# Kernel tuning notes

Measured on AMD Instinct MI355X. Metric: run time of the kernel, lower is better.

## Reference

```python
import jax
import jax.numpy as jnp
import numpy as np
from jax import lax

B, L, A, C = 32, 128, 64, 128  # batch, length, n_agents, channels (in == out)
KT = 3                          # temporal kernel size, padding (KT-1)//2 keeps length


def setup_inputs() -> dict:
    key = jax.random.key(0)
    k1, k2, k3 = jax.random.split(key, 3)
    x = jax.random.normal(k1, (B, L, A, C), dtype=jnp.float32)
    # Conv2d weight [out_ch, in_ch, kt, 1] and bias, kaiming-ish scale
    W = jax.random.normal(k2, (C, C, KT, 1), dtype=jnp.float32) * (1.0 / np.sqrt(C * KT))
    b = jax.random.normal(k3, (C,), dtype=jnp.float32) * 0.01
    return {"x": x, "W": W, "b": b}


def reference(x, W, b):
    # x: [B, L, A, C] -> [B, C, L, A] (torch NCHW layout with H=time, W=agents)
    length, n_agents = x.shape[1], x.shape[2]
    xc = jnp.transpose(x, (0, 3, 1, 2))
    res = xc  # residual is identity (input_dim == output_dim, t_stride == 1)
    pad_t = (KT - 1) // 2
    y = lax.conv_general_dilated(
        xc, W,
        window_strides=(1, 1),
        padding=[(pad_t, pad_t), (0, 0)],
        dimension_numbers=("NCHW", "OIHW", "NCHW"),
    ) + b[None, :, None, None]  # [B, C, L, A]
    # Dense graph g[t,a,t',a'] = 1 iff t==t' or a==a'.  einsum('ncv,vw->ncw', x, g)
    # is exactly: sum over same time (all agents) + sum over same agent (all times) - self.
    agent_sum = jnp.sum(y, axis=3, keepdims=True)  # [B, C, L, 1]
    time_sum = jnp.sum(y, axis=2, keepdims=True)   # [B, C, 1, A]
    scale = (length + n_agents - 2) ** 0.5
    g = (agent_sum + time_sum - y) / scale
    out = jax.nn.relu(g + res)
    return jnp.transpose(out, (0, 2, 3, 1))  # [B, L, A, C]
```

## Files before the change

kernel.cpp:

```cpp
#include <hip/hip_runtime.h>
#include <hip/hip_bf16.h>
#include <stdint.h>


typedef __attribute__((ext_vector_type(8))) short bf16x8;
typedef __attribute__((ext_vector_type(4))) float f32x4;

__device__ __forceinline__ uint32_t f2bf(float f) {
    union { __hip_bfloat16 b; uint16_t u; } cv;
    cv.b = __float2bfloat16(f);
    return (uint32_t)cv.u;
}
__device__ __forceinline__ float bf2f(uint32_t h) {
    union { uint32_t u; float f; } v; v.u = h << 16; return v.f;
}
__device__ __forceinline__ uint32_t pk2(float lo, float hi) {
    union { __hip_bfloat162 b; uint32_t u; } cv;
    cv.b = __float22bfloat162_rn(make_float2(lo, hi));
    return cv.u;
}

__global__ __launch_bounds__(256) void red_kernel(
    const float* __restrict__ x, uint16_t* __restrict__ xa16, float* __restrict__ xt_part,
    const float* __restrict__ W, uint16_t* __restrict__ wp)
{
    const int tid = threadIdx.x;
    const int bid = blockIdx.x;
    if (bid >= 512) {
        int o = (bid - 512) * 256 + tid;
        int i = o & 7, lane = (o >> 3) & 63, nt = (o >> 9) & 7, ks = (o >> 12) & 3, d = o >> 14;
        int ci = ks * 32 + (lane >> 4) * 8 + i;
        int co = nt * 16 + (lane & 15);
        wp[o] = (uint16_t)f2bf(W[(co * 128 + ci) * 3 + d]);
        return;
    }
    const int b = bid >> 4, g = bid & 15;
    const int ci8 = (tid & 15) * 8, ag = tid >> 4;
    __shared__ float red[16][128];

    float xtl[4][8];
    #pragma unroll
    for (int r = 0; r < 4; ++r)
        #pragma unroll
        for (int j = 0; j < 8; ++j) xtl[r][j] = 0.f;

    #pragma unroll
    for (int ti = 0; ti < 8; ++ti) {
        const int t = g * 8 + ti;
        const float* xr = x + ((size_t)(b * 128 + t) * 64) * 128;
        float s[8];
        #pragma unroll
        for (int j = 0; j < 8; ++j) s[j] = 0.f;
        #pragma unroll
        for (int r = 0; r < 4; ++r) {
            const int a = ag * 4 + r;
            const float4 v0 = *(const float4*)(xr + a * 128 + ci8);
            const float4 v1 = *(const float4*)(xr + a * 128 + ci8 + 4);
            s[0] += v0.x; s[1] += v0.y; s[2] += v0.z; s[3] += v0.w;
            s[4] += v1.x; s[5] += v1.y; s[6] += v1.z; s[7] += v1.w;
            xtl[r][0] += v0.x; xtl[r][1] += v0.y; xtl[r][2] += v0.z; xtl[r][3] += v0.w;
            xtl[r][4] += v1.x; xtl[r][5] += v1.y; xtl[r][6] += v1.z; xtl[r][7] += v1.w;
        }
        *(float4*)&red[ag][ci8]     = make_float4(s[0], s[1], s[2], s[3]);
        *(float4*)&red[ag][ci8 + 4] = make_float4(s[4], s[5], s[6], s[7]);
        __syncthreads();
        if (tid < 128) {
            float v = 0.f;
            #pragma unroll
            for (int i = 0; i < 16; ++i) v += red[i][tid];
            xa16[(size_t)(b * 130 + t + 1) * 128 + tid] = (uint16_t)f2bf(v);
        }
        __syncthreads();
    }
    if (g == 0 && tid < 16)
        *(uint4*)(xa16 + (size_t)(b * 130) * 128 + tid * 8) = make_uint4(0, 0, 0, 0);
    if (g == 15 && tid < 16)
        *(uint4*)(xa16 + (size_t)(b * 130 + 129) * 128 + tid * 8) = make_uint4(0, 0, 0, 0);
    #pragma unroll
    for (int r = 0; r < 4; ++r) {
        float* p = xt_part + (((size_t)(b * 16 + g) * 64 + ag * 4 + r) * 128) + ci8;
        *(float4*)p       = make_float4(xtl[r][0], xtl[r][1], xtl[r][2], xtl[r][3]);
        *(float4*)(p + 4) = make_float4(xtl[r][4], xtl[r][5], xtl[r][6], xtl[r][7]);
    }
}

__global__ __launch_bounds__(256) void xtr_kernel(
    const float* __restrict__ xt_part, float* __restrict__ xt)
{
    const int idx = blockIdx.x * 256 + threadIdx.x;
    const int row = idx >> 4, ci8 = (idx & 15) * 8;
    const int b = row >> 6, a = row & 63;
    float s[8];
    #pragma unroll
    for (int j = 0; j < 8; ++j) s[j] = 0.f;
    #pragma unroll
    for (int g2 = 0; g2 < 16; ++g2) {
        const float* p = xt_part + (((size_t)(b * 16 + g2) * 64 + a) * 128) + ci8;
        const float4 v0 = *(const float4*)p;
        const float4 v1 = *(const float4*)(p + 4);
        s[0] += v0.x; s[1] += v0.y; s[2] += v0.z; s[3] += v0.w;
        s[4] += v1.x; s[5] += v1.y; s[6] += v1.z; s[7] += v1.w;
    }
    float* q = xt + (size_t)row * 128 + ci8;
    *(float4*)q       = make_float4(s[0], s[1], s[2], s[3]);
    *(float4*)(q + 4) = make_float4(s[4], s[5], s[6], s[7]);
}

__global__ __launch_bounds__(256, 2) void sums_kernel(
    const uint16_t* __restrict__ xa16, const float* __restrict__ xt,
    const float* __restrict__ x, const uint16_t* __restrict__ wp,
    const float* __restrict__ bias, float* __restrict__ asum, float* __restrict__ tsum)
{
    __shared__ __align__(16) uint16_t slab[130 * 128];
    const int tid = threadIdx.x;
    const int lane = tid & 63, wid = tid >> 6;
    const int wm = wid >> 1, wn = wid & 1;
    const int lr = lane & 15, lg = lane >> 4;
    f32x4 acc[4][4];
    #pragma unroll
    for (int mi = 0; mi < 4; ++mi)
        #pragma unroll
        for (int ni = 0; ni < 4; ++ni) acc[mi][ni] = (f32x4)0.f;

    if (blockIdx.x < 32) {
        const int b = blockIdx.x;
        #pragma unroll
        for (int it = 0; it < 9; ++it) {
            const int gg = it * 256 + tid;
            if (gg < 2080) {
                const int row = gg >> 4, sp = gg & 15;
                const int sl = sp ^ (row & 7);
                *(uint4*)(slab + gg * 8) =
                    *(const uint4*)(xa16 + (size_t)(b * 130 + row) * 128 + sl * 8);
            }
        }
        __syncthreads();
        #pragma unroll
        for (int g = 0; g < 4; ++g)
            #pragma unroll
            for (int d = 0; d < 3; ++d) {
                bf16x8 bq[4], af[4];
                #pragma unroll
                for (int ni = 0; ni < 4; ++ni)
                    bq[ni] = *(const bf16x8*)(wp + (size_t)((((d * 4 + g) * 8) + wn * 4 + ni) * 64 + lane) * 8);
                #pragma unroll
                for (int mi = 0; mi < 4; ++mi) {
                    const int row = wm * 64 + mi * 16 + lr + d;
                    af[mi] = *(const bf16x8*)(slab + row * 128 + ((g * 4 + lg) ^ (row & 7)) * 8);
                }
                #pragma unroll
                for (int mi = 0; mi < 4; ++mi)
                    #pragma unroll
                    for (int ni = 0; ni < 4; ++ni)
                        acc[mi][ni] = __builtin_amdgcn_mfma_f32_16x16x32_bf16(af[mi], bq[ni], acc[mi][ni], 0, 0, 0);
            }
        #pragma unroll
        for (int ni = 0; ni < 4; ++ni) {
            const int col = wn * 64 + ni * 16 + lr;
            const float bv = 64.f * bias[col];
            #pragma unroll
            for (int mi = 0; mi < 4; ++mi)
                #pragma unroll
                for (int j = 0; j < 4; ++j) {
                    const int t = wm * 64 + mi * 16 + lg * 4 + j;
                    asum[((size_t)b * 128 + t) * 128 + col] = acc[mi][ni][j] + bv;
                }
        }
        return;
    }

    const int bid = blockIdx.x - 32;
    const int r = tid >> 1, h = tid & 1;
    const int grow = bid * 128 + r, sb = grow >> 6, sa = grow & 63;
    #pragma unroll
    for (int d = 0; d < 3; ++d) {
        {
            const float* Sp = xt + (size_t)grow * 128 + h * 64;
            const float* Ep = x + ((size_t)((sb * 128 + (d == 0 ? 127 : 0)) * 64 + sa)) * 128 + h * 64;
            #pragma unroll
            for (int k = 0; k < 8; ++k) {
                float4 f0 = *(const float4*)(Sp + k * 8);
                float4 f1 = *(const float4*)(Sp + k * 8 + 4);
                if (d != 1) {
                    const float4 e0 = *(const float4*)(Ep + k * 8);
                    const float4 e1 = *(const float4*)(Ep + k * 8 + 4);
                    f0.x -= e0.x; f0.y -= e0.y; f0.z -= e0.z; f0.w -= e0.w;
                    f1.x -= e1.x; f1.y -= e1.y; f1.z -= e1.z; f1.w -= e1.w;
                }
                uint4 o;
                o.x = pk2(f0.x, f0.y); o.y = pk2(f0.z, f0.w);
                o.z = pk2(f1.x, f1.y); o.w = pk2(f1.z, f1.w);
                const int sl = h * 8 + k;
                *(uint4*)(slab + r * 128 + (sl ^ (r & 7)) * 8) = o;
            }
        }
        __syncthreads();
        #pragma unroll
        for (int g = 0; g < 4; ++g) {
            bf16x8 bq[4], af[4];
            #pragma unroll
            for (int ni = 0; ni < 4; ++ni)
                bq[ni] = *(const bf16x8*)(wp + (size_t)((((d * 4 + g) * 8) + wn * 4 + ni) * 64 + lane) * 8);
            #pragma unroll
            for (int mi = 0; mi < 4; ++mi) {
                const int row = wm * 64 + mi * 16 + lr;
                af[mi] = *(const bf16x8*)(slab + row * 128 + ((g * 4 + lg) ^ (row & 7)) * 8);
            }
            #pragma unroll
            for (int mi = 0; mi < 4; ++mi)
                #pragma unroll
                for (int ni = 0; ni < 4; ++ni)
                    acc[mi][ni] = __builtin_amdgcn_mfma_f32_16x16x32_bf16(af[mi], bq[ni], acc[mi][ni], 0, 0, 0);
        }
        __syncthreads();
    }
    #pragma unroll
    for (int ni = 0; ni < 4; ++ni) {
        const int col = wn * 64 + ni * 16 + lr;
        const float bv = 128.f * bias[col];
        #pragma unroll
        for (int mi = 0; mi < 4; ++mi)
            #pragma unroll
            for (int j = 0; j < 4; ++j) {
                const int rg = bid * 128 + wm * 64 + mi * 16 + lg * 4 + j;
                tsum[(size_t)rg * 128 + col] = acc[mi][ni][j] + bv;
            }
    }
}

__global__ __launch_bounds__(512, 6) void conv_kernel(
    const float* __restrict__ x, const uint16_t* __restrict__ wp,
    const float* __restrict__ bias, const float* __restrict__ asum,
    const float* __restrict__ tsum, float* __restrict__ out)
{
    __shared__ __align__(16) uint16_t slab[2][192 * 64];
    const int tid = threadIdx.x;
    const int raw = blockIdx.x;
    const int bid = (raw & 7) * 512 + (raw >> 3);
    const int b = bid >> 7, t = bid & 127;
    const int lane = tid & 63, wid = tid >> 6;
    const int lr = lane & 15, lg = lane >> 4;

    f32x4 acc[4];
    #pragma unroll
    for (int mi = 0; mi < 4; ++mi) acc[mi] = (f32x4)0.f;

#define STAGE(c) do {                                                          \
    _Pragma("unroll")                                                          \
    for (int k = 0; k < 3; ++k) {                                              \
        const int ro  = lane >> 3;                                             \
        const int row = wid * 24 + k * 8 + ro;                                 \
        const int gl  = (lane & 7) ^ ro;                                       \
        const int tloc = t + (row >> 6) - 1;                                   \
        uint4 o4 = make_uint4(0, 0, 0, 0);                                     \
        if ((unsigned)tloc < 128u) {                                           \
            const float* s_ = x +                                              \
                ((size_t)((b * 128 + tloc) * 64 + (row & 63))) * 128 +         \
                (c) * 64 + gl * 8;                                             \
            const float4 v0 = *(const float4*)s_;                              \
            const float4 v1 = *(const float4*)(s_ + 4);                        \
            o4.x = pk2(v0.x, v0.y); o4.y = pk2(v0.z, v0.w);                    \
            o4.z = pk2(v1.x, v1.y); o4.w = pk2(v1.z, v1.w);                    \
        }                                                                      \
        *(uint4*)(&slab[c][wid * 1536 + k * 512 + lane * 8]) = o4;             \
    } } while (0)

#define MFMA_CHUNK(c) do {                                                     \
    _Pragma("unroll")                                                          \
    for (int d = 0; d < 3; ++d)                                                \
        _Pragma("unroll")                                                      \
        for (int g2 = 0; g2 < 2; ++g2) {                                       \
            const int ks = (c) * 2 + g2;                                       \
            bf16x8 bq, af[4];                                                  \
            bq = *(const bf16x8*)(wp +                                         \
                (size_t)((((d * 4 + ks) * 8) + wid) * 64 + lane) * 8);         \
            _Pragma("unroll")                                                  \
            for (int mi = 0; mi < 4; ++mi) {                                   \
                const int row = d * 64 + mi * 16 + lr;                         \
                af[mi] = *(const bf16x8*)(&slab[c][row * 64 +                  \
                    (((g2 * 4 + lg) ^ (row & 7)) * 8)]);                       \
            }                                                                  \
            _Pragma("unroll")                                                  \
            for (int mi = 0; mi < 4; ++mi)                                     \
                acc[mi] = __builtin_amdgcn_mfma_f32_16x16x32_bf16(             \
                    af[mi], bq, acc[mi], 0, 0, 0);                             \
        } } while (0)

    STAGE(0);
    __syncthreads();
    STAGE(1);
    MFMA_CHUNK(0);
    __syncthreads();
    MFMA_CHUNK(1);
    __syncthreads();

#undef STAGE
#undef MFMA_CHUNK

    {
        const int col = wid * 16 + lr;
        const float bv = bias[col];
        const int cbuf = col >> 6, cl = col & 63;
        #pragma unroll
        for (int mi = 0; mi < 4; ++mi)
            #pragma unroll
            for (int j = 0; j < 4; ++j) {
                const int a = mi * 16 + lg * 4 + j;
                slab[cbuf][a * 64 + (cl ^ ((a & 7) << 3))] = (uint16_t)f2bf(acc[mi][j] + bv);
            }
    }
    __syncthreads();

    {
        const float inv = 0.07254762501100116f;
        const int cg = tid & 15, rb = tid >> 4;
        const int cbuf = cg >> 3, cl8 = (cg & 7) * 8;
        const float* ap = asum + ((size_t)(b * 128 + t)) * 128 + cg * 8;
        const float4 as0 = *(const float4*)ap, as1 = *(const float4*)(ap + 4);
        const float av[8] = {as0.x, as0.y, as0.z, as0.w, as1.x, as1.y, as1.z, as1.w};
        #pragma unroll
        for (int j = 0; j < 2; ++j) {
            const int a = j * 32 + rb;
            const int swz = cl8 ^ ((a & 7) << 3);
            const uint4 yv = *(const uint4*)(&slab[cbuf][a * 64 + swz]);
            const uint4 xv = *(const uint4*)(&slab[cbuf][(64 + a) * 64 + swz]);
            const float* tp = tsum + ((size_t)(b * 64 + a)) * 128 + cg * 8;
            const float4 ts0 = *(const float4*)tp, ts1 = *(const float4*)(tp + 4);
            float yy[8], xx[8];
            yy[0] = bf2f(yv.x & 0xFFFFu); yy[1] = bf2f(yv.x >> 16);
            yy[2] = bf2f(yv.y & 0xFFFFu); yy[3] = bf2f(yv.y >> 16);
            yy[4] = bf2f(yv.z & 0xFFFFu); yy[5] = bf2f(yv.z >> 16);
            yy[6] = bf2f(yv.w & 0xFFFFu); yy[7] = bf2f(yv.w >> 16);
            xx[0] = bf2f(xv.x & 0xFFFFu); xx[1] = bf2f(xv.x >> 16);
            xx[2] = bf2f(xv.y & 0xFFFFu); xx[3] = bf2f(xv.y >> 16);
            xx[4] = bf2f(xv.z & 0xFFFFu); xx[5] = bf2f(xv.z >> 16);
            xx[6] = bf2f(xv.w & 0xFFFFu); xx[7] = bf2f(xv.w >> 16);
            const float tv[8] = {ts0.x, ts0.y, ts0.z, ts0.w, ts1.x, ts1.y, ts1.z, ts1.w};
            float o[8];
            #pragma unroll
            for (int i = 0; i < 8; ++i) {
                const float gg = (av[i] + tv[i] - yy[i]) * inv + xx[i];
                o[i] = gg > 0.f ? gg : 0.f;
            }
            float* op = out + ((size_t)((b * 128 + t) * 64 + a)) * 128 + cg * 8;
            *(float4*)op       = make_float4(o[0], o[1], o[2], o[3]);
            *(float4*)(op + 4) = make_float4(o[4], o[5], o[6], o[7]);
        }
    }
}

extern "C" void kernel_launch(void* const* d_in, const int* in_sizes, int n_in,
                              void* d_out, int out_size, void* d_ws, size_t ws_size,
                              hipStream_t stream) {
    const float* x    = (const float*)d_in[0];
    const float* W    = (const float*)d_in[1];
    const float* bias = (const float*)d_in[2];
    float* out = (float*)d_out;

    char* ws = (char*)d_ws;
    uint16_t* wp    = (uint16_t*)(ws);
    uint16_t* xa16  = (uint16_t*)(ws + 98304);
    float* xt_part  = (float*)(ws + 98304 + 1064960);
    float* xt       = (float*)(ws + 98304 + 1064960 + 16777216);
    float* asum     = (float*)(ws + 98304 + 1064960 + 16777216 + 1048576);
    float* tsum     = (float*)(ws + 98304 + 1064960 + 16777216 + 1048576 + 2097152);

    red_kernel  <<<704,  256, 0, stream>>>(x, xa16, xt_part, W, wp);
    xtr_kernel  <<<128,  256, 0, stream>>>(xt_part, xt);
    sums_kernel <<<48,   256, 0, stream>>>(xa16, xt, x, wp, bias, asum, tsum);
    conv_kernel <<<4096, 512, 0, stream>>>(x, wp, bias, asum, tsum, out);
}
```

Measured before the change: 109.8 us.

## Compute agent sums inside conv kernel and halve its LDS footprint

Drops the separate agent-sum path: the per-time reduction in red_kernel and the 32 MFMA blocks in sums_kernel go away. conv_kernel now gets the agent sum for each (b,t) by reducing its own accumulators across lanes with shuffles, writing it to a small shared array. The double-buffered LDS slab becomes a single buffer, with staging and MFMA serialized, so occupancy can rise from 6 to 8. The residual for the first channel half is reread from global x at full precision, because its bf16 copy has been overwritten. Serializing stage and compute gives up the overlap between loads and MFMA.

```diff
diff --git a/kernel.cpp b/kernel.cpp
--- a/kernel.cpp
+++ b/kernel.cpp
@@ -21,7 +21,7 @@
 }
 
 __global__ __launch_bounds__(256) void red_kernel(
-    const float* __restrict__ x, uint16_t* __restrict__ xa16, float* __restrict__ xt_part,
+    const float* __restrict__ x, float* __restrict__ xt_part,
     const float* __restrict__ W, uint16_t* __restrict__ wp)
 {
     const int tid = threadIdx.x;
@@ -36,7 +36,6 @@
     }
     const int b = bid >> 4, g = bid & 15;
     const int ci8 = (tid & 15) * 8, ag = tid >> 4;
-    __shared__ float red[16][128];
 
     float xtl[4][8];
     #pragma unroll
@@ -48,34 +47,15 @@
     for (int ti = 0; ti < 8; ++ti) {
         const int t = g * 8 + ti;
         const float* xr = x + ((size_t)(b * 128 + t) * 64) * 128;
-        float s[8];
-        #pragma unroll
-        for (int j = 0; j < 8; ++j) s[j] = 0.f;
         #pragma unroll
         for (int r = 0; r < 4; ++r) {
             const int a = ag * 4 + r;
             const float4 v0 = *(const float4*)(xr + a * 128 + ci8);
             const float4 v1 = *(const float4*)(xr + a * 128 + ci8 + 4);
-            s[0] += v0.x; s[1] += v0.y; s[2] += v0.z; s[3] += v0.w;
-            s[4] += v1.x; s[5] += v1.y; s[6] += v1.z; s[7] += v1.w;
             xtl[r][0] += v0.x; xtl[r][1] += v0.y; xtl[r][2] += v0.z; xtl[r][3] += v0.w;
             xtl[r][4] += v1.x; xtl[r][5] += v1.y; xtl[r][6] += v1.z; xtl[r][7] += v1.w;
         }
-        *(float4*)&red[ag][ci8]     = make_float4(s[0], s[1], s[2], s[3]);
-        *(float4*)&red[ag][ci8 + 4] = make_float4(s[4], s[5], s[6], s[7]);
-        __syncthreads();
-        if (tid < 128) {
-            float v = 0.f;
-            #pragma unroll
-            for (int i = 0; i < 16; ++i) v += red[i][tid];
-            xa16[(size_t)(b * 130 + t + 1) * 128 + tid] = (uint16_t)f2bf(v);
-        }
-        __syncthreads();
-    }
-    if (g == 0 && tid < 16)
-        *(uint4*)(xa16 + (size_t)(b * 130) * 128 + tid * 8) = make_uint4(0, 0, 0, 0);
-    if (g == 15 && tid < 16)
-        *(uint4*)(xa16 + (size_t)(b * 130 + 129) * 128 + tid * 8) = make_uint4(0, 0, 0, 0);
+    }
     #pragma unroll
     for (int r = 0; r < 4; ++r) {
         float* p = xt_part + (((size_t)(b * 16 + g) * 64 + ag * 4 + r) * 128) + ci8;
@@ -107,11 +87,11 @@
 }
 
 __global__ __launch_bounds__(256, 2) void sums_kernel(
-    const uint16_t* __restrict__ xa16, const float* __restrict__ xt,
-    const float* __restrict__ x, const uint16_t* __restrict__ wp,
-    const float* __restrict__ bias, float* __restrict__ asum, float* __restrict__ tsum)
+    const float* __restrict__ xt, const float* __restrict__ x,
+    const uint16_t* __restrict__ wp, const float* __restrict__ bias,
+    float* __restrict__ tsum)
 {
-    __shared__ __align__(16) uint16_t slab[130 * 128];
+    __shared__ __align__(16) uint16_t slab[128 * 128];
     const int tid = threadIdx.x;
     const int lane = tid & 63, wid = tid >> 6;
     const int wm = wid >> 1, wn = wid & 1;
@@ -122,54 +102,7 @@
         #pragma unroll
         for (int ni = 0; ni < 4; ++ni) acc[mi][ni] = (f32x4)0.f;
 
-    if (blockIdx.x < 32) {
-        const int b = blockIdx.x;
-        #pragma unroll
-        for (int it = 0; it < 9; ++it) {
-            const int gg = it * 256 + tid;
-            if (gg < 2080) {
-                const int row = gg >> 4, sp = gg & 15;
-                const int sl = sp ^ (row & 7);
-                *(uint4*)(slab + gg * 8) =
-                    *(const uint4*)(xa16 + (size_t)(b * 130 + row) * 128 + sl * 8);
-            }
-        }
-        __syncthreads();
-        #pragma unroll
-        for (int g = 0; g < 4; ++g)
-            #pragma unroll
-            for (int d = 0; d < 3; ++d) {
-                bf16x8 bq[4], af[4];
-                #pragma unroll
-                for (int ni = 0; ni < 4; ++ni)
-                    bq[ni] = *(const bf16x8*)(wp + (size_t)((((d * 4 + g) * 8) + wn * 4 + ni) * 64 + lane) * 8);
-                #pragma unroll
-                for (int mi = 0; mi < 4; ++mi) {
-                    const int row = wm * 64 + mi * 16 + lr + d;
-                    af[mi] = *(const bf16x8*)(slab + row * 128 + ((g * 4 + lg) ^ (row & 7)) * 8);
-                }
-                #pragma unroll
-                for (int mi = 0; mi < 4; ++mi)
-                    #pragma unroll
-                    for (int ni = 0; ni < 4; ++ni)
-                        acc[mi][ni] = __builtin_amdgcn_mfma_f32_16x16x32_bf16(af[mi], bq[ni], acc[mi][ni], 0, 0, 0);
-            }
-        #pragma unroll
-        for (int ni = 0; ni < 4; ++ni) {
-            const int col = wn * 64 + ni * 16 + lr;
-            const float bv = 64.f * bias[col];
-            #pragma unroll
-            for (int mi = 0; mi < 4; ++mi)
-                #pragma unroll
-                for (int j = 0; j < 4; ++j) {
-                    const int t = wm * 64 + mi * 16 + lg * 4 + j;
-                    asum[((size_t)b * 128 + t) * 128 + col] = acc[mi][ni][j] + bv;
-                }
-        }
-        return;
-    }
-
-    const int bid = blockIdx.x - 32;
+    const int bid = blockIdx.x;
     const int r = tid >> 1, h = tid & 1;
     const int grow = bid * 128 + r, sb = grow >> 6, sa = grow & 63;
     #pragma unroll
@@ -228,12 +161,13 @@
     }
 }
 
-__global__ __launch_bounds__(512, 6) void conv_kernel(
+__global__ __launch_bounds__(512, 8) void conv_kernel(
     const float* __restrict__ x, const uint16_t* __restrict__ wp,
-    const float* __restrict__ bias, const float* __restrict__ asum,
-    const float* __restrict__ tsum, float* __restrict__ out)
+    const float* __restrict__ bias, const float* __restrict__ tsum,
+    float* __restrict__ out)
 {
-    __shared__ __align__(16) uint16_t slab[2][192 * 64];
+    __shared__ __align__(16) uint16_t slab[192 * 64];
+    __shared__ __align__(16) float asl[128];
     const int tid = threadIdx.x;
     const int raw = blockIdx.x;
     const int bid = (raw & 7) * 512 + (raw >> 3);
@@ -262,7 +196,7 @@
             o4.x = pk2(v0.x, v0.y); o4.y = pk2(v0.z, v0.w);                    \
             o4.z = pk2(v1.x, v1.y); o4.w = pk2(v1.z, v1.w);                    \
         }                                                                      \
-        *(uint4*)(&slab[c][wid * 1536 + k * 512 + lane * 8]) = o4;             \
+        *(uint4*)(&slab[wid * 1536 + k * 512 + lane * 8]) = o4;                \
     } } while (0)
 
 #define MFMA_CHUNK(c) do {                                                     \
@@ -277,7 +211,7 @@
             _Pragma("unroll")                                                  \
             for (int mi = 0; mi < 4; ++mi) {                                   \
                 const int row = d * 64 + mi * 16 + lr;                         \
-                af[mi] = *(const bf16x8*)(&slab[c][row * 64 +                  \
+                af[mi] = *(const bf16x8*)(&slab[row * 64 +                     \
                     (((g2 * 4 + lg) ^ (row & 7)) * 8)]);                       \
             }                                                                  \
             _Pragma("unroll")                                                  \
@@ -288,25 +222,39 @@
 
     STAGE(0);
     __syncthreads();
+    MFMA_CHUNK(0);
+    __syncthreads();
     STAGE(1);
-    MFMA_CHUNK(0);
     __syncthreads();
     MFMA_CHUNK(1);
     __syncthreads();
 
 #undef STAGE
 #undef MFMA_CHUNK
+
+    {
+        float p = 0.f;
+        #pragma unroll
+        for (int mi = 0; mi < 4; ++mi)
+            #pragma unroll
+            for (int j = 0; j < 4; ++j) p += acc[mi][j];
+        p += __shfl_xor(p, 16);
+        p += __shfl_xor(p, 32);
+        const int col = wid * 16 + lr;
+        if (lg == 0) asl[col] = p + 64.f * bias[col];
+    }
 
     {
         const int col = wid * 16 + lr;
         const float bv = bias[col];
-        const int cbuf = col >> 6, cl = col & 63;
+        const int cl = col & 63;
+        const int rbase = (col >> 6) << 7;
         #pragma unroll
         for (int mi = 0; mi < 4; ++mi)
             #pragma unroll
             for (int j = 0; j < 4; ++j) {
                 const int a = mi * 16 + lg * 4 + j;
-                slab[cbuf][a * 64 + (cl ^ ((a & 7) << 3))] = (uint16_t)f2bf(acc[mi][j] + bv);
+                slab[(rbase + a) * 64 + (cl ^ ((a & 7) << 3))] = (uint16_t)f2bf(acc[mi][j] + bv);
             }
     }
     __syncthreads();
@@ -314,28 +262,38 @@
     {
         const float inv = 0.07254762501100116f;
         const int cg = tid & 15, rb = tid >> 4;
-        const int cbuf = cg >> 3, cl8 = (cg & 7) * 8;
-        const float* ap = asum + ((size_t)(b * 128 + t)) * 128 + cg * 8;
-        const float4 as0 = *(const float4*)ap, as1 = *(const float4*)(ap + 4);
+        const int cl8 = (cg & 7) * 8;
+        const float4 as0 = *(const float4*)(asl + cg * 8);
+        const float4 as1 = *(const float4*)(asl + cg * 8 + 4);
         const float av[8] = {as0.x, as0.y, as0.z, as0.w, as1.x, as1.y, as1.z, as1.w};
         #pragma unroll
         for (int j = 0; j < 2; ++j) {
             const int a = j * 32 + rb;
             const int swz = cl8 ^ ((a & 7) << 3);
-            const uint4 yv = *(const uint4*)(&slab[cbuf][a * 64 + swz]);
-            const uint4 xv = *(const uint4*)(&slab[cbuf][(64 + a) * 64 + swz]);
+            uint4 yv;
+            float xx[8];
+            if (cg < 8) {
+                yv = *(const uint4*)(&slab[a * 64 + swz]);
+                const float* xp = x + ((size_t)((b * 128 + t) * 64 + a)) * 128 + cg * 8;
+                const float4 x0 = *(const float4*)xp, x1 = *(const float4*)(xp + 4);
+                xx[0] = x0.x; xx[1] = x0.y; xx[2] = x0.z; xx[3] = x0.w;
+                xx[4] = x1.x; xx[5] = x1.y; xx[6] = x1.z; xx[7] = x1.w;
+            } else {
+                yv = *(const uint4*)(&slab[(128 + a) * 64 + swz]);
+                const uint4 xv = *(const uint4*)(&slab[(64 + a) * 64 + swz]);
+                xx[0] = bf2f(xv.x & 0xFFFFu); xx[1] = bf2f(xv.x >> 16);
+                xx[2] = bf2f(xv.y & 0xFFFFu); xx[3] = bf2f(xv.y >> 16);
+                xx[4] = bf2f(xv.z & 0xFFFFu); xx[5] = bf2f(xv.z >> 16);
+                xx[6] = bf2f(xv.w & 0xFFFFu); xx[7] = bf2f(xv.w >> 16);
+            }
             const float* tp = tsum + ((size_t)(b * 64 + a)) * 128 + cg * 8;
             const float4 ts0 = *(const float4*)tp, ts1 = *(const float4*)(tp + 4);
-            float yy[8], xx[8];
+            const float tv[8] = {ts0.x, ts0.y, ts0.z, ts0.w, ts1.x, ts1.y, ts1.z, ts1.w};
+            float yy[8];
             yy[0] = bf2f(yv.x & 0xFFFFu); yy[1] = bf2f(yv.x >> 16);
             yy[2] = bf2f(yv.y & 0xFFFFu); yy[3] = bf2f(yv.y >> 16);
             yy[4] = bf2f(yv.z & 0xFFFFu); yy[5] = bf2f(yv.z >> 16);
             yy[6] = bf2f(yv.w & 0xFFFFu); yy[7] = bf2f(yv.w >> 16);
-            xx[0] = bf2f(xv.x & 0xFFFFu); xx[1] = bf2f(xv.x >> 16);
-            xx[2] = bf2f(xv.y & 0xFFFFu); xx[3] = bf2f(xv.y >> 16);
-            xx[4] = bf2f(xv.z & 0xFFFFu); xx[5] = bf2f(xv.z >> 16);
-            xx[6] = bf2f(xv.w & 0xFFFFu); xx[7] = bf2f(xv.w >> 16);
-            const float tv[8] = {ts0.x, ts0.y, ts0.z, ts0.w, ts1.x, ts1.y, ts1.z, ts1.w};
             float o[8];
             #pragma unroll
             for (int i = 0; i < 8; ++i) {
@@ -359,14 +317,12 @@
 
     char* ws = (char*)d_ws;
     uint16_t* wp    = (uint16_t*)(ws);
-    uint16_t* xa16  = (uint16_t*)(ws + 98304);
-    float* xt_part  = (float*)(ws + 98304 + 1064960);
-    float* xt       = (float*)(ws + 98304 + 1064960 + 16777216);
-    float* asum     = (float*)(ws + 98304 + 1064960 + 16777216 + 1048576);
-    float* tsum     = (float*)(ws + 98304 + 1064960 + 16777216 + 1048576 + 2097152);
-
-    red_kernel  <<<704,  256, 0, stream>>>(x, xa16, xt_part, W, wp);
+    float* xt_part  = (float*)(ws + 98304);
+    float* xt       = (float*)(ws + 98304 + 16777216);
+    float* tsum     = (float*)(ws + 98304 + 16777216 + 1048576);
+
+    red_kernel  <<<704,  256, 0, stream>>>(x, xt_part, W, wp);
     xtr_kernel  <<<128,  256, 0, stream>>>(xt_part, xt);
-    sums_kernel <<<48,   256, 0, stream>>>(xa16, xt, x, wp, bias, asum, tsum);
-    conv_kernel <<<4096, 512, 0, stream>>>(x, wp, bias, asum, tsum, out);
-}
+    sums_kernel <<<16,   256, 0, stream>>>(xt, x, wp, bias, tsum);
+    conv_kernel <<<4096, 512, 0, stream>>>(x, wp, bias, tsum, out);
+}
```

New measurement: 116.0 us. 1.06x slower.
